# Kernel tuning notes

Measured on AMD Instinct MI355X. Metric: run time of the kernel, lower is better.

Reference implementation:

```python
import jax, jax.numpy as jnp
import numpy as np
from jax import lax

WINDOW_SIZE = 11
SIGMA = 1.5
CHANNELS = 3


def _gaussian_window():
    # 2D gaussian kernel, normalized to sum 1, shape [C, 1, K, K] (OIHW depthwise)
    coords = jnp.arange(WINDOW_SIZE, dtype=jnp.float32) - WINDOW_SIZE // 2
    g2d = jnp.exp(-(coords[None, :] ** 2 + coords[:, None] ** 2) / (2.0 * SIGMA ** 2))
    g2d = g2d / g2d.sum()
    return jnp.broadcast_to(g2d[None, None], (CHANNELS, 1, WINDOW_SIZE, WINDOW_SIZE))


def _depthwise_blur(x, window):
    pad = WINDOW_SIZE // 2
    return lax.conv_general_dilated(
        x, window,
        window_strides=(1, 1),
        padding=[(pad, pad), (pad, pad)],
        dimension_numbers=("NCHW", "OIHW", "NCHW"),
        feature_group_count=CHANNELS,
    )


def setup_inputs() -> dict:
    key = jax.random.key(0)
    k1, k2 = jax.random.split(key)
    shape = (16, 3, 512, 512)
    img1 = jax.random.uniform(k1, shape, dtype=jnp.float32)
    img2 = jax.random.uniform(k2, shape, dtype=jnp.float32)
    return {"img1": img1, "img2": img2}


def reference(img1, img2):
    window = _gaussian_window()
    C1 = 0.01 ** 2
    C2 = 0.03 ** 2

    mu1 = _depthwise_blur(img1, window)
    mu2 = _depthwise_blur(img2, window)
    mu1_sq = mu1 * mu1
    mu2_sq = mu2 * mu2
    mu1_mu2 = mu1 * mu2

    sigma1_sq = _depthwise_blur(img1 * img1, window) - mu1_sq
    sigma2_sq = _depthwise_blur(img2 * img2, window) - mu2_sq
    sigma12 = _depthwise_blur(img1 * img2, window) - mu1_mu2

    ssim_map = ((2.0 * mu1_mu2 + C1) * (2.0 * sigma12 + C2)) / (
        (mu1_sq + mu2_sq + C1) * (sigma1_sq + sigma2_sq + C2)
    )
    # size_average=True -> scalar loss
    return 1.0 - ssim_map.mean()
```

## Files before the change

### kernel.cpp

```cpp
#include <hip/hip_runtime.h>

#define IMG 512
#define PAD 5
#define KW  11
#define SH  64
#define WCOLS 64
#define NWAVES 4
#define BW (WCOLS * NWAVES)
#define STG (WCOLS + 2 * PAD)
#define NPLANES 48
#define NCHUNK 7

typedef float v2f __attribute__((ext_vector_type(2)));

__global__ __launch_bounds__(256, 2) void ssim_pk_kernel(
    const float* __restrict__ img1,
    const float* __restrict__ img2,
    double* __restrict__ accum)
{
    __shared__ v2f sbuf[NWAVES][STG + 1];

#define W0 0.00102837f
#define W1 0.00759874f
#define W2 0.03600077f
#define W3 0.10936370f
#define W4 0.21300551f
#define W5 0.26601172f
    static constexpr float WK[KW] = {W0, W1, W2, W3, W4, W5, W4, W3, W2, W1, W0};

    const int tid   = threadIdx.x;
    const int wv_id = tid >> 6;
    const int lane  = tid & 63;
    const int plane = blockIdx.z;
    const int wc0   = blockIdx.x * BW + wv_id * WCOLS;
    const int y0    = blockIdx.y * SH;

    const float* __restrict__ A = img1 + (size_t)plane * (IMG * IMG);
    const float* __restrict__ B = img2 + (size_t)plane * (IMG * IMG);
    v2f* lbuf = &sbuf[wv_id][0];

    const int c0  = wc0 - PAD + lane;
    const int cc0 = min(max(c0, 0), IMG - 1);
    const float m0 = (c0 >= 0 && c0 < IMG) ? 1.f : 0.f;
    const int c1  = wc0 + (WCOLS - PAD) + lane;
    const int cc1 = min(c1, IMG - 1);
    const float m1 = (c1 < IMG) ? 1.f : 0.f;

    const int ystart = max(y0 - PAD, 0);
    const int yend   = min(y0 + SH + PAD, IMG);

    v2f rmu[KW], rx[KW];
#pragma unroll
    for (int j = 0; j < KW; ++j) {
        rmu[j] = (v2f)0.f;
        rx[j]  = (v2f)0.f;
    }

    const float C1v = 1e-4f;
    const float C2v = 9e-4f;
    float local = 0.f;

    const float* rowA = A + (size_t)ystart * IMG;
    const float* rowB = B + (size_t)ystart * IMG;
    float pa0 = rowA[cc0], pb0 = rowB[cc0];
    float pa1 = rowA[cc1], pb1 = rowB[cc1];

    int y = ystart;

#define SSIM_EMIT(sd)                                                          \
    {                                                                          \
        const float mu1 = rmu[sd].x, mu2 = rmu[sd].y;                          \
        const float xs  = rx[sd].x,  x2ab = rx[sd].y;        \
        const float m12 = mu1 * mu2;                                           \
        const float t2m = m12 + m12;                                           \
        const float num = (t2m + C1v) * ((x2ab - t2m) + C2v);                  \
        const float ssum = fmaf(mu1, mu1, mu2 * mu2);                          \
        const float den = (ssum + C1v) * ((xs - ssum) + C2v);                  \
        local += num * __builtin_amdgcn_rcpf(den);                             \
    }

#define SSIM_PHASE(p)                                                          \
    if (y < yend) {                                                            \
                  \
        {                                                                      \
            v2f st; st.x = pa0 * m0; st.y = pb0 * m0;                          \
            lbuf[lane] = st;                                                   \
            if (lane < 2 * PAD) {                                              \
                v2f se; se.x = pa1 * m1; se.y = pb1 * m1;                      \
                lbuf[WCOLS + lane] = se;                                       \
            }                                                                  \
        }                                                                      \
               \
        if (y + 1 < yend) {                                                    \
            rowA += IMG; rowB += IMG;                                          \
            pa0 = rowA[cc0]; pb0 = rowB[cc0];                                  \
            pa1 = rowA[cc1]; pb1 = rowB[cc1];                                  \
        }                                                                      \
                                     \
        v2f hmu = (v2f)0.f, hx = (v2f)0.f;                                     \
        _Pragma("unroll")                                                      \
        for (int k = 0; k < KW; ++k) {                                         \
            const v2f ab = lbuf[lane + k];                       \
            v2f aa;  aa.x = ab.x;  aa.y = ab.x;                  \
            v2f byy; byy.x = ab.y; byy.y = ab.y;                 \
            v2f byx; byx.x = ab.y; byx.y = ab.x;                 \
            v2f u = aa * ab;                                     \
            u = byy * byx + u;                               \
            const v2f wk2 = {WK[k], WK[k]};                                    \
            hmu = wk2 * ab + hmu;                                              \
            hx  = wk2 * u  + hx;                                               \
        }                                                                      \
           \
        _Pragma("unroll")                                                      \
        for (int j = 0; j < KW; ++j) {                                         \
            const int sl = ((p) + 6 + j) % KW;                                 \
            const v2f wj2 = {WK[j], WK[j]};     \
            rmu[sl] = wj2 * hmu + rmu[sl];                                     \
            rx[sl]  = wj2 * hx  + rx[sl];                                      \
        }                                                                      \
                                        \
        {                                                                      \
            const int sd = ((p) + 6) % KW;                                     \
            const int r = y - PAD;                                             \
            if (r >= y0) SSIM_EMIT(sd);                                        \
            rmu[sd] = (v2f)0.f;                                                \
            rx[sd]  = (v2f)0.f;                                                \
        }                                                                      \
        ++y;                                                                   \
    }

#pragma unroll 1
    for (int chunk = 0; chunk < NCHUNK; ++chunk) {
        SSIM_PHASE(0) SSIM_PHASE(1) SSIM_PHASE(2) SSIM_PHASE(3)
        SSIM_PHASE(4) SSIM_PHASE(5) SSIM_PHASE(6) SSIM_PHASE(7)
        SSIM_PHASE(8) SSIM_PHASE(9) SSIM_PHASE(10)
    }
#undef SSIM_PHASE

    if (blockIdx.y == (IMG / SH - 1)) {
        SSIM_EMIT(9) SSIM_EMIT(10) SSIM_EMIT(0) SSIM_EMIT(1) SSIM_EMIT(2)
    }
#undef SSIM_EMIT

#pragma unroll
    for (int off = 32; off > 0; off >>= 1)
        local += __shfl_down(local, off);
    if (lane == 0)
        atomicAdd(accum, (double)local);
}

__global__ void ssim_finalize_kernel(const double* __restrict__ accum,
                                     float* __restrict__ out)
{
    const double N = (double)NPLANES * IMG * IMG;
    out[0] = (float)(1.0 - accum[0] / N);
}

extern "C" void kernel_launch(void* const* d_in, const int* in_sizes, int n_in,
                              void* d_out, int out_size, void* d_ws, size_t ws_size,
                              hipStream_t stream) {
    const float* img1 = (const float*)d_in[0];
    const float* img2 = (const float*)d_in[1];
    float* out = (float*)d_out;
    double* accum = (double*)d_ws;

    hipMemsetAsync(accum, 0, sizeof(double), stream);

    dim3 grid(IMG / BW, IMG / SH, NPLANES);
    ssim_pk_kernel<<<grid, BW, 0, stream>>>(img1, img2, accum);
    ssim_finalize_kernel<<<1, 1, 0, stream>>>(accum, out);
}
```

Before: 175.8 us.

## Halve row strip height, double-buffer row prefetch, and spread atomics over slots

Row strips shrink from 64 to 32 rows, which doubles the grid and raises occupancy through a waves_per_eu hint. Row loads now come from two alternating register sets, prefetching two rows ahead instead of one. The per-wave atomic is replaced by a block-level LDS reduction and one atomic per block spread across 64 double slots, which a 64-thread finalize kernel then sums. The price is more halo recomputation (42 rows processed per 32 output) and a __syncthreads at the end of each block.

```diff
diff --git a/kernel.cpp b/kernel.cpp
--- a/kernel.cpp
+++ b/kernel.cpp
@@ -3,22 +3,25 @@
 #define IMG 512
 #define PAD 5
 #define KW  11
-#define SH  64
+#define SH  32
 #define WCOLS 64
 #define NWAVES 4
 #define BW (WCOLS * NWAVES)
 #define STG (WCOLS + 2 * PAD)
 #define NPLANES 48
-#define NCHUNK 7
+#define NSLOTS 64
 
 typedef float v2f __attribute__((ext_vector_type(2)));
 
-__global__ __launch_bounds__(256, 2) void ssim_pk_kernel(
+__global__
+__attribute__((amdgpu_flat_work_group_size(256, 256), amdgpu_waves_per_eu(4)))
+void ssim_pk32_kernel(
     const float* __restrict__ img1,
     const float* __restrict__ img2,
     double* __restrict__ accum)
 {
     __shared__ v2f sbuf[NWAVES][STG + 1];
+    __shared__ float wsum[NWAVES];
 
 #define W0 0.00102837f
 #define W1 0.00759874f
@@ -60,10 +63,16 @@
     const float C2v = 9e-4f;
     float local = 0.f;
 
-    const float* rowA = A + (size_t)ystart * IMG;
-    const float* rowB = B + (size_t)ystart * IMG;
-    float pa0 = rowA[cc0], pb0 = rowB[cc0];
-    float pa1 = rowA[cc1], pb1 = rowB[cc1];
+    float xa0, xb0, xa1, xb1, ya0, yb0, ya1, yb1;
+    {
+        const size_t r0 = (size_t)ystart * IMG;
+        xa0 = A[r0 + cc0]; xb0 = B[r0 + cc0];
+        xa1 = A[r0 + cc1]; xb1 = B[r0 + cc1];
+        const int y1c = min(ystart + 1, yend - 1);
+        const size_t r1 = (size_t)y1c * IMG;
+        ya0 = A[r1 + cc0]; yb0 = B[r1 + cc0];
+        ya1 = A[r1 + cc1]; yb1 = B[r1 + cc1];
+    }
 
     int y = ystart;
 
@@ -79,22 +88,21 @@
         local += num * __builtin_amdgcn_rcpf(den);                             \
     }
 
-#define SSIM_PHASE(p)                                                          \
+#define SSIM_PHASE(p, CA0, CB0, CA1, CB1)                                      \
     if (y < yend) {                                                            \
-                  \
-        {                                                                      \
-            v2f st; st.x = pa0 * m0; st.y = pb0 * m0;                          \
+        {               \
+            v2f st; st.x = CA0 * m0; st.y = CB0 * m0;                          \
             lbuf[lane] = st;                                                   \
             if (lane < 2 * PAD) {                                              \
-                v2f se; se.x = pa1 * m1; se.y = pb1 * m1;                      \
+                v2f se; se.x = CA1 * m1; se.y = CB1 * m1;                      \
                 lbuf[WCOLS + lane] = se;                                       \
             }                                                                  \
         }                                                                      \
-               \
-        if (y + 1 < yend) {                                                    \
-            rowA += IMG; rowB += IMG;                                          \
-            pa0 = rowA[cc0]; pb0 = rowB[cc0];                                  \
-            pa1 = rowA[cc1]; pb1 = rowB[cc1];                                  \
+        {                   \
+            int yy = y + 2; if (yy > yend - 1) yy = yend - 1;                  \
+            const size_t ro = (size_t)yy * IMG;                                \
+            CA0 = A[ro + cc0]; CB0 = B[ro + cc0];                              \
+            CA1 = A[ro + cc1]; CB1 = B[ro + cc1];                              \
         }                                                                      \
                                      \
         v2f hmu = (v2f)0.f, hx = (v2f)0.f;                                     \
@@ -130,30 +138,50 @@
     }
 
 #pragma unroll 1
-    for (int chunk = 0; chunk < NCHUNK; ++chunk) {
-        SSIM_PHASE(0) SSIM_PHASE(1) SSIM_PHASE(2) SSIM_PHASE(3)
-        SSIM_PHASE(4) SSIM_PHASE(5) SSIM_PHASE(6) SSIM_PHASE(7)
-        SSIM_PHASE(8) SSIM_PHASE(9) SSIM_PHASE(10)
+    for (int chunk = 0; chunk < 2; ++chunk) {
+        SSIM_PHASE(0,  xa0, xb0, xa1, xb1)  SSIM_PHASE(1,  ya0, yb0, ya1, yb1)
+        SSIM_PHASE(2,  xa0, xb0, xa1, xb1)  SSIM_PHASE(3,  ya0, yb0, ya1, yb1)
+        SSIM_PHASE(4,  xa0, xb0, xa1, xb1)  SSIM_PHASE(5,  ya0, yb0, ya1, yb1)
+        SSIM_PHASE(6,  xa0, xb0, xa1, xb1)  SSIM_PHASE(7,  ya0, yb0, ya1, yb1)
+        SSIM_PHASE(8,  xa0, xb0, xa1, xb1)  SSIM_PHASE(9,  ya0, yb0, ya1, yb1)
+        SSIM_PHASE(10, xa0, xb0, xa1, xb1)  SSIM_PHASE(11, ya0, yb0, ya1, yb1)
+        SSIM_PHASE(12, xa0, xb0, xa1, xb1)  SSIM_PHASE(13, ya0, yb0, ya1, yb1)
+        SSIM_PHASE(14, xa0, xb0, xa1, xb1)  SSIM_PHASE(15, ya0, yb0, ya1, yb1)
+        SSIM_PHASE(16, xa0, xb0, xa1, xb1)  SSIM_PHASE(17, ya0, yb0, ya1, yb1)
+        SSIM_PHASE(18, xa0, xb0, xa1, xb1)  SSIM_PHASE(19, ya0, yb0, ya1, yb1)
+        SSIM_PHASE(20, xa0, xb0, xa1, xb1)  SSIM_PHASE(21, ya0, yb0, ya1, yb1)
     }
 #undef SSIM_PHASE
 
     if (blockIdx.y == (IMG / SH - 1)) {
-        SSIM_EMIT(9) SSIM_EMIT(10) SSIM_EMIT(0) SSIM_EMIT(1) SSIM_EMIT(2)
+        SSIM_EMIT(10) SSIM_EMIT(0) SSIM_EMIT(1) SSIM_EMIT(2) SSIM_EMIT(3)
     }
 #undef SSIM_EMIT
 
 #pragma unroll
     for (int off = 32; off > 0; off >>= 1)
         local += __shfl_down(local, off);
-    if (lane == 0)
-        atomicAdd(accum, (double)local);
+    if (lane == 0) wsum[wv_id] = local;
+    __syncthreads();
+    if (tid == 0) {
+        const float bs = wsum[0] + wsum[1] + wsum[2] + wsum[3];
+        const int slot = (int)(((blockIdx.z * gridDim.y + blockIdx.y) * gridDim.x
+                                + blockIdx.x) & (NSLOTS - 1));
+        atomicAdd(&accum[slot], (double)bs);
+    }
 }
 
 __global__ void ssim_finalize_kernel(const double* __restrict__ accum,
                                      float* __restrict__ out)
 {
-    const double N = (double)NPLANES * IMG * IMG;
-    out[0] = (float)(1.0 - accum[0] / N);
+    double v = accum[threadIdx.x];
+#pragma unroll
+    for (int off = 32; off > 0; off >>= 1)
+        v += __shfl_down(v, off);
+    if (threadIdx.x == 0) {
+        const double N = (double)NPLANES * IMG * IMG;
+        out[0] = (float)(1.0 - v / N);
+    }
 }
 
 extern "C" void kernel_launch(void* const* d_in, const int* in_sizes, int n_in,
@@ -164,9 +192,9 @@
     float* out = (float*)d_out;
     double* accum = (double*)d_ws;
 
-    hipMemsetAsync(accum, 0, sizeof(double), stream);
+    hipMemsetAsync(accum, 0, NSLOTS * sizeof(double), stream);
 
     dim3 grid(IMG / BW, IMG / SH, NPLANES);
-    ssim_pk_kernel<<<grid, BW, 0, stream>>>(img1, img2, accum);
-    ssim_finalize_kernel<<<1, 1, 0, stream>>>(accum, out);
+    ssim_pk32_kernel<<<grid, BW, 0, stream>>>(img1, img2, accum);
+    ssim_finalize_kernel<<<1, 64, 0, stream>>>(accum, out);
 }
```

Result: faster. 159.6 us (-9.2%).
